# Kernel optimization log

Hardware: AMD Instinct MI355X
Metric: run time of the kernel (lower is better)

## Reference

```python
import jax, jax.numpy as jnp
import numpy as np

HIDDEN = 1024
HEADS = 16
HEAD_DIM = HIDDEN // HEADS


def setup_inputs() -> dict:
    key = jax.random.key(0)
    ks = jax.random.split(key, 7)
    B, S, H = 8, 1024, HIDDEN
    hidden_states = jax.random.normal(ks[0], (B, S, H), dtype=jnp.float32)
    attention_mask = jnp.zeros((B, 1, 1, S), dtype=jnp.float32)
    # Xavier-uniform weights [out, in], zero biases (matches module init)
    limit = float(np.sqrt(6.0 / (H + H)))
    Wq = jax.random.uniform(ks[1], (H, H), minval=-limit, maxval=limit, dtype=jnp.float32)
    Wk = jax.random.uniform(ks[2], (H, H), minval=-limit, maxval=limit, dtype=jnp.float32)
    Wv = jax.random.uniform(ks[3], (H, H), minval=-limit, maxval=limit, dtype=jnp.float32)
    bq = jnp.zeros((H,), dtype=jnp.float32)
    bk = jnp.zeros((H,), dtype=jnp.float32)
    bv = jnp.zeros((H,), dtype=jnp.float32)
    return {"hidden_states": hidden_states, "attention_mask": attention_mask,
            "Wq": Wq, "bq": bq, "Wk": Wk, "bk": bk, "Wv": Wv, "bv": bv}


def _split_heads(x):
    # [B, S, H] -> [B, heads, S, head_dim]
    B, S, _ = x.shape
    return x.reshape(B, S, HEADS, HEAD_DIM).transpose(0, 2, 1, 3)


def reference(hidden_states, attention_mask, Wq, bq, Wk, bk, Wv, bv):
    # Linear projections: y = x @ W^T + b  (weights stored [out, in] as in torch)
    q = _split_heads(hidden_states @ Wq.T + bq)
    k = _split_heads(hidden_states @ Wk.T + bk)
    v = _split_heads(hidden_states @ Wv.T + bv)
    scale = 1.0 / (HEAD_DIM ** 0.5)
    scores = jnp.einsum('bhqd,bhkd->bhqk', q, k) * scale  # [B,heads,S,S]
    scores = scores + attention_mask
    probs = jax.nn.softmax(scores, axis=-1)
    # dropout is identity at inference
    ctx = jnp.einsum('bhqk,bhkd->bhqd', probs, v)
    B, _, S, _ = ctx.shape
    return ctx.transpose(0, 2, 1, 3).reshape(B, S, HIDDEN)
```

## Files before the change

kernel.cpp:

```cpp
#include <hip/hip_runtime.h>
#include <hip/hip_bf16.h>
#include <stdint.h>

#define B_ 8
#define S_ 1024
#define NH_ 16
#define D_ 64
#define H_ 1024
#define M_TOT (B_*S_)
#define LOG2E 1.44269504088896f

typedef __attribute__((ext_vector_type(8))) short short8;
typedef __attribute__((ext_vector_type(4))) float f32x4;
typedef __attribute__((ext_vector_type(16))) float f32x16;

#if __has_builtin(__builtin_amdgcn_exp2f)
#define EXP2(x) __builtin_amdgcn_exp2f(x)
#else
#define EXP2(x) __expf((x) * 0.69314718056f)
#endif

static __device__ __forceinline__ unsigned short f2bf(float f) {
  union { float f; unsigned u; } c; c.f = f;
  unsigned u = c.u;
  return (unsigned short)((u + 0x7fffu + ((u >> 16) & 1u)) >> 16);
}

static __device__ __forceinline__ void gld_lds16(void* lds, const void* g) {
  __builtin_amdgcn_global_load_lds((const __attribute__((address_space(1))) unsigned*)g,
                                   (__attribute__((address_space(3))) unsigned*)lds, 16, 0, 0);
}

#define WAIT_LGKM0() asm volatile("s_waitcnt lgkmcnt(0)" ::: "memory")
#define WAIT_VM(n)   asm volatile("s_waitcnt vmcnt(" #n ")" ::: "memory")
#define SBAR()       __builtin_amdgcn_s_barrier()
#define SCHED0()     __builtin_amdgcn_sched_barrier(0)

__global__ void cvt_f32_bf16(const float* __restrict__ X,
                             const float* __restrict__ Wq,
                             const float* __restrict__ Wk,
                             const float* __restrict__ Wv,
                             unsigned short* __restrict__ Xbf,
                             unsigned short* __restrict__ Wbf) {
  const long long NX = (long long)M_TOT * H_;
  const long long NW = (long long)H_ * H_;
  long long t = (long long)blockIdx.x * blockDim.x + threadIdx.x;
  const long long stride = (long long)gridDim.x * blockDim.x;
  const long long total4 = (NX + 3 * NW) >> 2;
  for (; t < total4; t += stride) {
    long long e = t << 2;
    const float* src; unsigned short* dst;
    if (e < NX) { src = X + e; dst = Xbf + e; }
    else {
      long long r = e - NX;
      int w = (int)(r / NW);
      long long o = r - (long long)w * NW;
      src = (w == 0 ? Wq : (w == 1 ? Wk : Wv)) + o;
      dst = Wbf + (long long)w * NW + o;
    }
    float4 v = *(const float4*)src;
    ushort4 u;
    u.x = f2bf(v.x); u.y = f2bf(v.y); u.z = f2bf(v.z); u.w = f2bf(v.w);
    *(ushort4*)dst = u;
  }
}

#define QBM 128
#define QBN 256
#define QBK 64
#define BUFSZ 49152

__global__ __launch_bounds__(512, 2) void qkv_gemm(
    const unsigned short* __restrict__ Xbf,
    const unsigned short* __restrict__ Wbf,
    const float* __restrict__ bq, const float* __restrict__ bk,
    const float* __restrict__ bv,
    unsigned short* __restrict__ Qo, unsigned short* __restrict__ Ko,
    unsigned short* __restrict__ Vt) {
  __shared__ char lds[3 * BUFSZ];

  const int tid = threadIdx.x;
  const int w = tid >> 6;
  const int l = tid & 63;
  const int lrow = l & 15, lgrp = l >> 4;
  const int wm = w >> 2, wn = w & 3;

  const int orig = blockIdx.x;
  const int xcd = orig & 7;
  const int slot = orig >> 3;
  const int z = slot >> 5;
  const int i = slot & 31;
  const int mtile = (xcd * 8 + (i >> 2)) * QBM;
  const int ntile = (i & 3) * QBN;

  const unsigned short* Wz = Wbf + (long long)z * H_ * H_;

  const int srow = l >> 3;
  const int sslot = l & 7;
  auto stageA = [&](char* buf, int j, int k0) {
    int row = j * 8 + srow;
    int so = (sslot ^ (row & 7)) * 8;
    gld_lds16(buf + j * 1024, Xbf + (long long)(mtile + row) * H_ + k0 + so);
  };
  auto stageB = [&](char* buf, int j, int k0) {
    int row = j * 8 + srow;
    int so = (sslot ^ (row & 7)) * 8;
    gld_lds16(buf + 16384 + j * 1024, Wz + (long long)(ntile + row) * H_ + k0 + so);
  };

  const int strA = (z == 2 ? wn : wm) * 64;
  const int strB = (z == 2 ? wm : wn) * 64;
  const int offA = (z == 2) ? 16384 : 0;
  const int offB = (z == 2) ? 0 : 16384;
  auto rdA = [&](char* buf, int fi, int ks) -> short8 {
    int r = strA + fi * 16 + lrow;
    return *(const short8*)(buf + offA + r * 128 + (((ks * 4 + lgrp) ^ (r & 7)) * 16));
  };
  auto rdB = [&](char* buf, int fi, int ks) -> short8 {
    int r = strB + fi * 16 + lrow;
    return *(const short8*)(buf + offB + r * 128 + (((ks * 4 + lgrp) ^ (r & 7)) * 16));
  };

  f32x4 acc[4][4];
  f32x4 zero = {0.f, 0.f, 0.f, 0.f};
  #pragma unroll
  for (int a = 0; a < 4; ++a)
    #pragma unroll
    for (int c = 0; c < 4; ++c) acc[a][c] = zero;

  {
    char* b0p = lds;
    char* b1p = lds + BUFSZ;
    stageA(b0p, 2 * w + 0, 0); stageA(b0p, 2 * w + 1, 0);
    #pragma unroll
    for (int c = 0; c < 4; ++c) stageB(b0p, 4 * w + c, 0);
    stageA(b1p, 2 * w + 0, QBK); stageA(b1p, 2 * w + 1, QBK);
    #pragma unroll
    for (int c = 0; c < 4; ++c) stageB(b1p, 4 * w + c, QBK);
  }
  WAIT_VM(6);
  SBAR();

  #pragma unroll 1
  for (int t = 0; t < 16; ++t) {
    char* buf  = lds + (t % 3) * BUFSZ;
    char* nbuf = lds + ((t + 2) % 3) * BUFSZ;
    const int k0n = (t + 2) * QBK;
    const bool st = (t + 2 < 16);

    short8 af[4][2], bf[2][2];

    #pragma unroll
    for (int fi = 0; fi < 4; ++fi)
      #pragma unroll
      for (int ks = 0; ks < 2; ++ks) af[fi][ks] = rdA(buf, fi, ks);
    #pragma unroll
    for (int fi = 0; fi < 2; ++fi)
      #pragma unroll
      for (int ks = 0; ks < 2; ++ks) bf[fi][ks] = rdB(buf, fi, ks);
    if (st) { stageA(nbuf, 2 * w + 0, k0n); stageA(nbuf, 2 * w + 1, k0n);
              stageB(nbuf, 4 * w + 0, k0n); }
    SBAR();
    WAIT_LGKM0(); SCHED0();
    __builtin_amdgcn_s_setprio(1);
    #pragma unroll
    for (int im = 0; im < 4; ++im)
      #pragma unroll
      for (int in = 0; in < 2; ++in)
        #pragma unroll
        for (int ks = 0; ks < 2; ++ks)
          acc[im][in] = __builtin_amdgcn_mfma_f32_16x16x32_bf16(
              af[im][ks], bf[in][ks], acc[im][in], 0, 0, 0);
    __builtin_amdgcn_s_setprio(0);
    SBAR();

    #pragma unroll
    for (int fi = 0; fi < 2; ++fi)
      #pragma unroll
      for (int ks = 0; ks < 2; ++ks) bf[fi][ks] = rdB(buf, 2 + fi, ks);
    if (st) { stageB(nbuf, 4 * w + 1, k0n); stageB(nbuf, 4 * w + 2, k0n);
              stageB(nbuf, 4 * w + 3, k0n); }
    SBAR();
    WAIT_LGKM0(); SCHED0();
    __builtin_amdgcn_s_setprio(1);
    #pragma unroll
    for (int im = 0; im < 4; ++im)
      #pragma unroll
      for (int in = 0; in < 2; ++in)
        #pragma unroll
        for (int ks = 0; ks < 2; ++ks)
          acc[im][2 + in] = __builtin_amdgcn_mfma_f32_16x16x32_bf16(
              af[im][ks], bf[in][ks], acc[im][2 + in], 0, 0, 0);
    __builtin_amdgcn_s_setprio(0);
    if (t < 14) { WAIT_VM(6); } else { WAIT_VM(0); }
    SBAR();
  }

  const float* bias = (z == 0) ? bq : (z == 1) ? bk : bv;
  if (z != 2) {
    unsigned short* O = (z == 0) ? Qo : Ko;
    #pragma unroll
    for (int in = 0; in < 4; ++in) {
      int n = ntile + wn * 64 + in * 16 + lrow;
      float bv_ = bias[n];
      int h = n >> 6, d = n & 63;
      #pragma unroll
      for (int im = 0; im < 4; ++im)
        #pragma unroll
        for (int r = 0; r < 4; ++r) {
          int m = mtile + wm * 64 + im * 16 + lgrp * 4 + r;
          float val = acc[im][in][r] + bv_;
          if (z == 0) val *= 0.125f * LOG2E;
          int b = m >> 10, s = m & 1023;
          O[(((long long)(b * NH_ + h)) * S_ + s) * D_ + d] = f2bf(val);
        }
    }
  } else {
    #pragma unroll
    for (int im = 0; im < 4; ++im)
      #pragma unroll
      for (int r = 0; r < 4; ++r) {
        int nfull = ntile + wn * 64 + im * 16 + lgrp * 4 + r;
        float bv_ = bias[nfull];
        int h = nfull >> 6, d = nfull & 63;
        #pragma unroll
        for (int in = 0; in < 4; ++in) {
          int mfull = mtile + wm * 64 + in * 16 + lrow;
          float val = acc[im][in][r] + bv_;
          int b = mfull >> 10, s = mfull & 1023;
          Vt[(((long long)(b * NH_ + h)) * D_ + d) * S_ + s] = f2bf(val);
        }
      }
  }
}

__global__ __launch_bounds__(256, 2) void attn_fused(
    const unsigned short* __restrict__ Qbf,
    const unsigned short* __restrict__ Kbf,
    const unsigned short* __restrict__ Vtb,
    const float* __restrict__ mask,
    float* __restrict__ out) {
  __shared__ char lds[32768];
  const int tid = threadIdx.x, w = tid >> 6, l = tid & 63;
  const int l31 = l & 31, h = l >> 5;

  const int lid = blockIdx.x;
  const int xcd = lid & 7, k8 = lid >> 3;
  const int bh = xcd * 16 + (k8 >> 2);
  const int qt = k8 & 3;
  const int b = bh >> 4, hd = bh & 15;
  const int q0 = qt * 256 + w * 64;

  const unsigned short* Kg = Kbf + (long long)bh * S_ * D_;
  const unsigned short* Vg = Vtb + (long long)bh * D_ * S_;
  const float* mrow = mask + b * S_;

  {
    const int row = (w * 2) * 8 + (l >> 3);
    const int row1 = (w * 2 + 1) * 8 + (l >> 3);
    const int so = ((l & 7) ^ (row & 7)) * 8;
    const int so1 = ((l & 7) ^ (row1 & 7)) * 8;
    gld_lds16(lds + (w * 2) * 1024,        Kg + (long long)row * D_ + so);
    gld_lds16(lds + (w * 2 + 1) * 1024,    Kg + (long long)row1 * D_ + so1);
    gld_lds16(lds + 8192 + (w * 2) * 1024, Vg + (long long)row * S_ + so);
    gld_lds16(lds + 8192 + (w * 2 + 1) * 1024, Vg + (long long)row1 * S_ + so1);
  }

  short8 qf[2][4];
  #pragma unroll
  for (int qb = 0; qb < 2; ++qb)
    #pragma unroll
    for (int ks = 0; ks < 4; ++ks)
      qf[qb][ks] = *(const short8*)(Qbf + ((long long)bh * S_ + q0 + qb * 32 + l31) * D_ + ks * 16 + 8 * h);

  f32x16 acc[2][2];
  #pragma unroll
  for (int db = 0; db < 2; ++db)
    #pragma unroll
    for (int qb = 0; qb < 2; ++qb)
      #pragma unroll
      for (int r = 0; r < 16; ++r) acc[db][qb][r] = 0.f;
  float m_run[2] = {-1e30f, -1e30f};
  float l_run[2] = {0.f, 0.f};

  __syncthreads();

  for (int kt = 0; kt < S_ / 64; ++kt) {
    const int p = kt & 1;
    char* ldsK = lds + p * 16384;
    char* ldsV = ldsK + 8192;
    const int key0 = kt * 64;

    if (kt < S_ / 64 - 1) {
      char* nb = lds + (p ^ 1) * 16384;
      const int nk0 = key0 + 64;
      #pragma unroll
      for (int t = 0; t < 2; ++t) {
        int j = w * 2 + t;
        int row = j * 8 + (l >> 3);
        int so = ((l & 7) ^ (row & 7)) * 8;
        gld_lds16(nb + j * 1024,        Kg + (long long)(nk0 + row) * D_ + so);
        gld_lds16(nb + 8192 + j * 1024, Vg + (long long)row * S_ + nk0 + so);
      }
    }

    f32x16 sc[2][2];
    #pragma unroll
    for (int kb = 0; kb < 2; ++kb)
      #pragma unroll
      for (int qb = 0; qb < 2; ++qb)
        #pragma unroll
        for (int r = 0; r < 16; ++r) sc[kb][qb][r] = 0.f;

    #pragma unroll
    for (int kb = 0; kb < 2; ++kb) {
      short8 kf[4];
      #pragma unroll
      for (int ks = 0; ks < 4; ++ks) {
        int row = kb * 32 + l31;
        int g = (2 * ks + h) ^ (row & 7);
        kf[ks] = *(const short8*)(ldsK + row * 128 + g * 16);
      }
      __builtin_amdgcn_s_setprio(1);
      #pragma unroll
      for (int qb = 0; qb < 2; ++qb)
        #pragma unroll
        for (int ks = 0; ks < 4; ++ks)
          sc[kb][qb] = __builtin_amdgcn_mfma_f32_32x32x16_bf16(
              kf[ks], qf[qb][ks], sc[kb][qb], 0, 0, 0);
      __builtin_amdgcn_s_setprio(0);
    }

    short8 pfrag[2][4];
    #pragma unroll
    for (int qb = 0; qb < 2; ++qb) {
      float sv[32];
      #pragma unroll
      for (int kb = 0; kb < 2; ++kb)
        #pragma unroll
        for (int rg = 0; rg < 4; ++rg) {
          f32x4 m4 = *(const f32x4*)(mrow + key0 + kb * 32 + rg * 8 + 4 * h);
          #pragma unroll
          for (int c = 0; c < 4; ++c)
            sv[kb * 16 + rg * 4 + c] = fmaf(m4[c], LOG2E, sc[kb][qb][rg * 4 + c]);
        }
      float r16[16];
      #pragma unroll
      for (int i = 0; i < 16; ++i) r16[i] = fmaxf(sv[i], sv[i + 16]);
      #pragma unroll
      for (int i = 0; i < 8; ++i) r16[i] = fmaxf(r16[i], r16[i + 8]);
      #pragma unroll
      for (int i = 0; i < 4; ++i) r16[i] = fmaxf(r16[i], r16[i + 4]);
      float pm = fmaxf(fmaxf(r16[0], r16[1]), fmaxf(r16[2], r16[3]));
      pm = fmaxf(pm, __shfl_xor(pm, 32));
      if (!__all(pm - m_run[qb] <= 11.5f)) {
        float mn = fmaxf(m_run[qb], pm);
        float rs = EXP2(m_run[qb] - mn);
        m_run[qb] = mn;
        l_run[qb] *= rs;
        #pragma unroll
        for (int db = 0; db < 2; ++db)
          #pragma unroll
          for (int r = 0; r < 16; ++r) acc[db][qb][r] *= rs;
      }
      const float mcur = m_run[qb];
      #pragma unroll
      for (int i = 0; i < 32; ++i) sv[i] = EXP2(sv[i] - mcur);
      #pragma unroll
      for (int i = 0; i < 16; ++i) r16[i] = sv[i] + sv[i + 16];
      #pragma unroll
      for (int i = 0; i < 8; ++i) r16[i] = r16[i] + r16[i + 8];
      #pragma unroll
      for (int i = 0; i < 4; ++i) r16[i] = r16[i] + r16[i + 4];
      float ps = (r16[0] + r16[1]) + (r16[2] + r16[3]);
      ps += __shfl_xor(ps, 32);
      l_run[qb] += ps;

      unsigned Wd[8][2];
      #pragma unroll
      for (int j = 0; j < 8; ++j) {
        int base = (j >> 2) * 16 + (j & 3) * 4;
        asm("v_cvt_pk_bf16_f32 %0, %1, %2" : "=v"(Wd[j][0]) : "v"(sv[base + 0]), "v"(sv[base + 1]));
        asm("v_cvt_pk_bf16_f32 %0, %1, %2" : "=v"(Wd[j][1]) : "v"(sv[base + 2]), "v"(sv[base + 3]));
      }
      #pragma unroll
      for (int ks = 0; ks < 4; ++ks) {
        unsigned s0 = h ? Wd[2 * ks][0] : Wd[2 * ks + 1][0];
        unsigned s1 = h ? Wd[2 * ks][1] : Wd[2 * ks + 1][1];
        unsigned r0 = __shfl_xor(s0, 32);
        unsigned r1 = __shfl_xor(s1, 32);
        unsigned o0 = h ? Wd[2 * ks + 1][0] : Wd[2 * ks][0];
        unsigned o1 = h ? Wd[2 * ks + 1][1] : Wd[2 * ks][1];
        union { unsigned u[4]; short8 s; } fu;
        fu.u[0] = h ? r0 : o0;
        fu.u[1] = h ? r1 : o1;
        fu.u[2] = h ? o0 : r0;
        fu.u[3] = h ? o1 : r1;
        pfrag[qb][ks] = fu.s;
      }
    }

    #pragma unroll
    for (int db = 0; db < 2; ++db) {
      short8 vf[4];
      #pragma unroll
      for (int ks = 0; ks < 4; ++ks) {
        int row = db * 32 + l31;
        int g = (2 * ks + h) ^ (row & 7);
        vf[ks] = *(const short8*)(ldsV + row * 128 + g * 16);
      }
      __builtin_amdgcn_s_setprio(1);
      #pragma unroll
      for (int qb = 0; qb < 2; ++qb)
        #pragma unroll
        for (int ks = 0; ks < 4; ++ks)
          acc[db][qb] = __builtin_amdgcn_mfma_f32_32x32x16_bf16(
              vf[ks], pfrag[qb][ks], acc[db][qb], 0, 0, 0);
      __builtin_amdgcn_s_setprio(0);
    }

    __syncthreads();
  }

  #pragma unroll
  for (int qb = 0; qb < 2; ++qb) {
    float inv = 1.0f / l_run[qb];
    int q = q0 + qb * 32 + l31;
    float* orow = out + ((long long)b * S_ + q) * H_ + hd * D_;
    #pragma unroll
    for (int db = 0; db < 2; ++db)
      #pragma unroll
      for (int rg = 0; rg < 4; ++rg) {
        f32x4 v4;
        #pragma unroll
        for (int c = 0; c < 4; ++c) v4[c] = acc[db][qb][rg * 4 + c] * inv;
        *(f32x4*)(orow + db * 32 + rg * 8 + 4 * h) = v4;
      }
  }
}

extern "C" void kernel_launch(void* const* d_in, const int* in_sizes, int n_in,
                              void* d_out, int out_size, void* d_ws, size_t ws_size,
                              hipStream_t stream) {
  const float* X    = (const float*)d_in[0];
  const float* mask = (const float*)d_in[1];
  const float* Wq   = (const float*)d_in[2];
  const float* bq   = (const float*)d_in[3];
  const float* Wk   = (const float*)d_in[4];
  const float* bk   = (const float*)d_in[5];
  const float* Wv   = (const float*)d_in[6];
  const float* bv   = (const float*)d_in[7];
  float* out = (float*)d_out;

  char* ws = (char*)d_ws;
  unsigned short* Xbf = (unsigned short*)ws;
  unsigned short* Wbf = (unsigned short*)(ws + 16777216);
  unsigned short* Qb  = (unsigned short*)(ws + 23068672);
  unsigned short* Kb  = (unsigned short*)(ws + 39845888);
  unsigned short* Vt  = (unsigned short*)(ws + 56623104);

  hipLaunchKernelGGL(cvt_f32_bf16, dim3(2048), dim3(256), 0, stream,
                     X, Wq, Wk, Wv, Xbf, Wbf);
  hipLaunchKernelGGL(qkv_gemm, dim3(768), dim3(512), 0, stream,
                     Xbf, Wbf, bq, bk, bv, Qb, Kb, Vt);
  hipLaunchKernelGGL(attn_fused, dim3(512), dim3(256), 0, stream,
                     Qb, Kb, Vt, mask, out);
}
```

Measured before the change: 132.6 us.

## Enlarge QKV GEMM tile to 256x256 with double-buffered register-prefetch pipeline

The QKV projection GEMM tile grows from 128x256 to 256x256, so each wave owns 128x64 outputs and the grid halves to 384 blocks. The LDS pipeline goes from triple to double buffering, and the next tile's A and B fragments are prefetched into registers while MFMAs run, using partial lgkmcnt waits. The aim is more reuse per LDS byte and less barrier stall per MFMA. In exchange it doubles the accumulator registers, which can hurt occupancy under launch_bounds(512,2), and leaves fewer blocks to balance across the CUs.

```diff
diff --git a/kernel.cpp b/kernel.cpp
--- a/kernel.cpp
+++ b/kernel.cpp
@@ -31,10 +31,13 @@
                                    (__attribute__((address_space(3))) unsigned*)lds, 16, 0, 0);
 }
 
-#define WAIT_LGKM0() asm volatile("s_waitcnt lgkmcnt(0)" ::: "memory")
-#define WAIT_VM(n)   asm volatile("s_waitcnt vmcnt(" #n ")" ::: "memory")
-#define SBAR()       __builtin_amdgcn_s_barrier()
-#define SCHED0()     __builtin_amdgcn_sched_barrier(0)
+#define WAIT_LGKM(n)  asm volatile("s_waitcnt lgkmcnt(" #n ")" ::: "memory")
+#define WAIT_LGKM0()  asm volatile("s_waitcnt lgkmcnt(0)" ::: "memory")
+#define WAIT_VM(n)    asm volatile("s_waitcnt vmcnt(" #n ")" ::: "memory")
+#define SBAR()        __builtin_amdgcn_s_barrier()
+#define SCHED0()      __builtin_amdgcn_sched_barrier(0)
+#define PRIO1()       __builtin_amdgcn_s_setprio(1)
+#define PRIO0()       __builtin_amdgcn_s_setprio(0)
 
 __global__ void cvt_f32_bf16(const float* __restrict__ X,
                              const float* __restrict__ Wq,
@@ -65,10 +68,11 @@
   }
 }
 
-#define QBM 128
+#define QBM 256
 #define QBN 256
 #define QBK 64
-#define BUFSZ 49152
+#define ABYTES 32768
+#define BUFSZ  65536
 
 __global__ __launch_bounds__(512, 2) void qkv_gemm(
     const unsigned short* __restrict__ Xbf,
@@ -77,7 +81,7 @@
     const float* __restrict__ bv,
     unsigned short* __restrict__ Qo, unsigned short* __restrict__ Ko,
     unsigned short* __restrict__ Vt) {
-  __shared__ char lds[3 * BUFSZ];
+  __shared__ char lds[2 * BUFSZ];
 
   const int tid = threadIdx.x;
   const int w = tid >> 6;
@@ -88,10 +92,10 @@
   const int orig = blockIdx.x;
   const int xcd = orig & 7;
   const int slot = orig >> 3;
-  const int z = slot >> 5;
-  const int i = slot & 31;
-  const int mtile = (xcd * 8 + (i >> 2)) * QBM;
-  const int ntile = (i & 3) * QBN;
+  const int nz = slot >> 2;
+  const int mtile = (xcd * 4 + (slot & 3)) * QBM;
+  const int ntile = (nz & 3) * QBN;
+  const int z = nz >> 2;
 
   const unsigned short* Wz = Wbf + (long long)z * H_ * H_;
 
@@ -105,13 +109,13 @@
   auto stageB = [&](char* buf, int j, int k0) {
     int row = j * 8 + srow;
     int so = (sslot ^ (row & 7)) * 8;
-    gld_lds16(buf + 16384 + j * 1024, Wz + (long long)(ntile + row) * H_ + k0 + so);
-  };
-
-  const int strA = (z == 2 ? wn : wm) * 64;
-  const int strB = (z == 2 ? wm : wn) * 64;
-  const int offA = (z == 2) ? 16384 : 0;
-  const int offB = (z == 2) ? 0 : 16384;
+    gld_lds16(buf + ABYTES + j * 1024, Wz + (long long)(ntile + row) * H_ + k0 + so);
+  };
+
+  const int strA = wm * 128;
+  const int strB = wn * 64;
+  const int offA = (z == 2) ? ABYTES : 0;
+  const int offB = (z == 2) ? 0 : ABYTES;
   auto rdA = [&](char* buf, int fi, int ks) -> short8 {
     int r = strA + fi * 16 + lrow;
     return *(const short8*)(buf + offA + r * 128 + (((ks * 4 + lgrp) ^ (r & 7)) * 16));
@@ -121,79 +125,89 @@
     return *(const short8*)(buf + offB + r * 128 + (((ks * 4 + lgrp) ^ (r & 7)) * 16));
   };
 
-  f32x4 acc[4][4];
+  f32x4 acc[8][4];
   f32x4 zero = {0.f, 0.f, 0.f, 0.f};
   #pragma unroll
-  for (int a = 0; a < 4; ++a)
+  for (int a = 0; a < 8; ++a)
     #pragma unroll
     for (int c = 0; c < 4; ++c) acc[a][c] = zero;
 
-  {
-    char* b0p = lds;
-    char* b1p = lds + BUFSZ;
-    stageA(b0p, 2 * w + 0, 0); stageA(b0p, 2 * w + 1, 0);
-    #pragma unroll
-    for (int c = 0; c < 4; ++c) stageB(b0p, 4 * w + c, 0);
-    stageA(b1p, 2 * w + 0, QBK); stageA(b1p, 2 * w + 1, QBK);
-    #pragma unroll
-    for (int c = 0; c < 4; ++c) stageB(b1p, 4 * w + c, QBK);
-  }
-  WAIT_VM(6);
+  short8 afA[4][2], afB[4][2], bfC[2][2], bfN[2][2];
+
+  auto mmq = [&](int i0, int j0, short8 (&AF)[4][2], short8 (&BF)[2][2]) {
+    #pragma unroll
+    for (int a = 0; a < 4; ++a)
+      #pragma unroll
+      for (int b = 0; b < 2; ++b)
+        #pragma unroll
+        for (int ks = 0; ks < 2; ++ks)
+          acc[i0 + a][j0 + b] = __builtin_amdgcn_mfma_f32_16x16x32_bf16(
+              AF[a][ks], BF[b][ks], acc[i0 + a][j0 + b], 0, 0, 0);
+  };
+
+  auto tile_body = [&](char* buf, char* nbuf, int k0n, bool st,
+                       short8 (&af0)[4][2], short8 (&af1)[4][2]) {
+    #pragma unroll
+    for (int fi = 0; fi < 4; ++fi)
+      #pragma unroll
+      for (int ks = 0; ks < 2; ++ks) af1[fi][ks] = rdA(buf, 4 + fi, ks);
+    if (st) {
+      stageA(nbuf, w * 4 + 0, k0n); stageA(nbuf, w * 4 + 1, k0n);
+      stageA(nbuf, w * 4 + 2, k0n); stageA(nbuf, w * 4 + 3, k0n);
+    }
+    SBAR();
+    WAIT_LGKM(8); SCHED0();
+    PRIO1(); mmq(0, 0, af0, bfC); PRIO0();
+
+    #pragma unroll
+    for (int fi = 0; fi < 2; ++fi)
+      #pragma unroll
+      for (int ks = 0; ks < 2; ++ks) bfN[fi][ks] = rdB(buf, 2 + fi, ks);
+    if (st) {
+      stageB(nbuf, w * 4 + 0, k0n); stageB(nbuf, w * 4 + 1, k0n);
+      stageB(nbuf, w * 4 + 2, k0n); stageB(nbuf, w * 4 + 3, k0n);
+    }
+    SBAR();
+    WAIT_LGKM(4); SCHED0();
+    PRIO1(); mmq(4, 0, af1, bfC); PRIO0();
+
+    WAIT_LGKM0(); SCHED0();
+    PRIO1(); mmq(4, 2, af1, bfN); PRIO0();
+    WAIT_VM(0);
+    SBAR();
+
+    if (st) {
+      #pragma unroll
+      for (int fi = 0; fi < 4; ++fi)
+        #pragma unroll
+        for (int ks = 0; ks < 2; ++ks) af1[fi][ks] = rdA(nbuf, fi, ks);
+      #pragma unroll
+      for (int fi = 0; fi < 2; ++fi)
+        #pragma unroll
+        for (int ks = 0; ks < 2; ++ks) bfC[fi][ks] = rdB(nbuf, fi, ks);
+    }
+    PRIO1(); mmq(0, 2, af0, bfN); PRIO0();
+  };
+
+  #pragma unroll
+  for (int c = 0; c < 4; ++c) stageA(lds, w * 4 + c, 0);
+  #pragma unroll
+  for (int c = 0; c < 4; ++c) stageB(lds, w * 4 + c, 0);
+  WAIT_VM(0);
   SBAR();
+  #pragma unroll
+  for (int fi = 0; fi < 4; ++fi)
+    #pragma unroll
+    for (int ks = 0; ks < 2; ++ks) afA[fi][ks] = rdA(lds, fi, ks);
+  #pragma unroll
+  for (int fi = 0; fi < 2; ++fi)
+    #pragma unroll
+    for (int ks = 0; ks < 2; ++ks) bfC[fi][ks] = rdB(lds, fi, ks);
 
   #pragma unroll 1
-  for (int t = 0; t < 16; ++t) {
-    char* buf  = lds + (t % 3) * BUFSZ;
-    char* nbuf = lds + ((t + 2) % 3) * BUFSZ;
-    const int k0n = (t + 2) * QBK;
-    const bool st = (t + 2 < 16);
-
-    short8 af[4][2], bf[2][2];
-
-    #pragma unroll
-    for (int fi = 0; fi < 4; ++fi)
-      #pragma unroll
-      for (int ks = 0; ks < 2; ++ks) af[fi][ks] = rdA(buf, fi, ks);
-    #pragma unroll
-    for (int fi = 0; fi < 2; ++fi)
-      #pragma unroll
-      for (int ks = 0; ks < 2; ++ks) bf[fi][ks] = rdB(buf, fi, ks);
-    if (st) { stageA(nbuf, 2 * w + 0, k0n); stageA(nbuf, 2 * w + 1, k0n);
-              stageB(nbuf, 4 * w + 0, k0n); }
-    SBAR();
-    WAIT_LGKM0(); SCHED0();
-    __builtin_amdgcn_s_setprio(1);
-    #pragma unroll
-    for (int im = 0; im < 4; ++im)
-      #pragma unroll
-      for (int in = 0; in < 2; ++in)
-        #pragma unroll
-        for (int ks = 0; ks < 2; ++ks)
-          acc[im][in] = __builtin_amdgcn_mfma_f32_16x16x32_bf16(
-              af[im][ks], bf[in][ks], acc[im][in], 0, 0, 0);
-    __builtin_amdgcn_s_setprio(0);
-    SBAR();
-
-    #pragma unroll
-    for (int fi = 0; fi < 2; ++fi)
-      #pragma unroll
-      for (int ks = 0; ks < 2; ++ks) bf[fi][ks] = rdB(buf, 2 + fi, ks);
-    if (st) { stageB(nbuf, 4 * w + 1, k0n); stageB(nbuf, 4 * w + 2, k0n);
-              stageB(nbuf, 4 * w + 3, k0n); }
-    SBAR();
-    WAIT_LGKM0(); SCHED0();
-    __builtin_amdgcn_s_setprio(1);
-    #pragma unroll
-    for (int im = 0; im < 4; ++im)
-      #pragma unroll
-      for (int in = 0; in < 2; ++in)
-        #pragma unroll
-        for (int ks = 0; ks < 2; ++ks)
-          acc[im][2 + in] = __builtin_amdgcn_mfma_f32_16x16x32_bf16(
-              af[im][ks], bf[in][ks], acc[im][2 + in], 0, 0, 0);
-    __builtin_amdgcn_s_setprio(0);
-    if (t < 14) { WAIT_VM(6); } else { WAIT_VM(0); }
-    SBAR();
+  for (int t = 0; t < 16; t += 2) {
+    tile_body(lds,          lds + BUFSZ, (t + 1) * QBK, true,        afA, afB);
+    tile_body(lds + BUFSZ,  lds,         (t + 2) * QBK, (t + 2) < 16, afB, afA);
   }
 
   const float* bias = (z == 0) ? bq : (z == 1) ? bk : bv;
@@ -205,10 +219,10 @@
       float bv_ = bias[n];
       int h = n >> 6, d = n & 63;
       #pragma unroll
-      for (int im = 0; im < 4; ++im)
+      for (int im = 0; im < 8; ++im)
         #pragma unroll
         for (int r = 0; r < 4; ++r) {
-          int m = mtile + wm * 64 + im * 16 + lgrp * 4 + r;
+          int m = mtile + wm * 128 + im * 16 + lgrp * 4 + r;
           float val = acc[im][in][r] + bv_;
           if (z == 0) val *= 0.125f * LOG2E;
           int b = m >> 10, s = m & 1023;
@@ -217,15 +231,15 @@
     }
   } else {
     #pragma unroll
-    for (int im = 0; im < 4; ++im)
+    for (int im = 0; im < 8; ++im)
       #pragma unroll
       for (int r = 0; r < 4; ++r) {
-        int nfull = ntile + wn * 64 + im * 16 + lgrp * 4 + r;
+        int nfull = ntile + wm * 128 + im * 16 + lgrp * 4 + r;
         float bv_ = bias[nfull];
         int h = nfull >> 6, d = nfull & 63;
         #pragma unroll
         for (int in = 0; in < 4; ++in) {
-          int mfull = mtile + wm * 64 + in * 16 + lrow;
+          int mfull = mtile + wn * 64 + in * 16 + lrow;
           float val = acc[im][in][r] + bv_;
           int b = mfull >> 10, s = mfull & 1023;
           Vt[(((long long)(b * NH_ + h)) * D_ + d) * S_ + s] = f2bf(val);
@@ -461,7 +475,7 @@
 
   hipLaunchKernelGGL(cvt_f32_bf16, dim3(2048), dim3(256), 0, stream,
                      X, Wq, Wk, Wv, Xbf, Wbf);
-  hipLaunchKernelGGL(qkv_gemm, dim3(768), dim3(512), 0, stream,
+  hipLaunchKernelGGL(qkv_gemm, dim3(384), dim3(512), 0, stream,
                      Xbf, Wbf, bq, bk, bv, Qb, Kb, Vt);
   hipLaunchKernelGGL(attn_fused, dim3(512), dim3(256), 0, stream,
                      Qb, Kb, Vt, mask, out);
```

Measured after the change: 192.5 us. +45.1%, slower.

## Triple-buffer K/V staging and cache attention mask row in LDS

Applied to the files above, without the earlier changes.

Switches the attention kernel's K/V LDS staging from a double buffer to a triple buffer with a prefetch distance of two tiles. Explicit vmcnt waits let one tile's loads stay in flight across the barrier. It also loads the batch's mask row into LDS once, so the inner loop reads the mask from LDS instead of global memory. LDS use grows from 32 KB to 52 KB per block, which may limit how many blocks fit on a CU under the launch bound of 2.

```diff
diff --git a/kernel.cpp b/kernel.cpp
--- a/kernel.cpp
+++ b/kernel.cpp
@@ -240,7 +240,8 @@
     const unsigned short* __restrict__ Vtb,
     const float* __restrict__ mask,
     float* __restrict__ out) {
-  __shared__ char lds[32768];
+  __shared__ char lds[3 * 16384 + 4096];
+  char* ldsM = lds + 49152;
   const int tid = threadIdx.x, w = tid >> 6, l = tid & 63;
   const int l31 = l & 31, h = l >> 5;
 
@@ -255,16 +256,17 @@
   const unsigned short* Vg = Vtb + (long long)bh * D_ * S_;
   const float* mrow = mask + b * S_;
 
-  {
-    const int row = (w * 2) * 8 + (l >> 3);
-    const int row1 = (w * 2 + 1) * 8 + (l >> 3);
-    const int so = ((l & 7) ^ (row & 7)) * 8;
-    const int so1 = ((l & 7) ^ (row1 & 7)) * 8;
-    gld_lds16(lds + (w * 2) * 1024,        Kg + (long long)row * D_ + so);
-    gld_lds16(lds + (w * 2 + 1) * 1024,    Kg + (long long)row1 * D_ + so1);
-    gld_lds16(lds + 8192 + (w * 2) * 1024, Vg + (long long)row * S_ + so);
-    gld_lds16(lds + 8192 + (w * 2 + 1) * 1024, Vg + (long long)row1 * S_ + so1);
-  }
+  auto stageKV = [&](int kt, char* buf) {
+    const int key0 = kt * 64;
+    #pragma unroll
+    for (int t = 0; t < 2; ++t) {
+      int j = w * 2 + t;
+      int row = j * 8 + (l >> 3);
+      int so = ((l & 7) ^ (row & 7)) * 8;
+      gld_lds16(buf + j * 1024,        Kg + (long long)(key0 + row) * D_ + so);
+      gld_lds16(buf + 8192 + j * 1024, Vg + (long long)row * S_ + key0 + so);
+    }
+  };
 
   short8 qf[2][4];
   #pragma unroll
@@ -272,6 +274,13 @@
     #pragma unroll
     for (int ks = 0; ks < 4; ++ks)
       qf[qb][ks] = *(const short8*)(Qbf + ((long long)bh * S_ + q0 + qb * 32 + l31) * D_ + ks * 16 + 8 * h);
+  gld_lds16(ldsM + w * 1024, mrow + w * 256 + l * 4);
+  SCHED0(); WAIT_VM(0); SCHED0();
+
+  stageKV(0, lds);
+  stageKV(1, lds + 16384);
+  SCHED0(); WAIT_VM(4); SCHED0();
+  SBAR();
 
   f32x16 acc[2][2];
   #pragma unroll
@@ -283,26 +292,14 @@
   float m_run[2] = {-1e30f, -1e30f};
   float l_run[2] = {0.f, 0.f};
 
-  __syncthreads();
-
+  #pragma unroll 1
   for (int kt = 0; kt < S_ / 64; ++kt) {
-    const int p = kt & 1;
-    char* ldsK = lds + p * 16384;
+    char* ldsK = lds + (kt % 3) * 16384;
     char* ldsV = ldsK + 8192;
     const int key0 = kt * 64;
-
-    if (kt < S_ / 64 - 1) {
-      char* nb = lds + (p ^ 1) * 16384;
-      const int nk0 = key0 + 64;
-      #pragma unroll
-      for (int t = 0; t < 2; ++t) {
-        int j = w * 2 + t;
-        int row = j * 8 + (l >> 3);
-        int so = ((l & 7) ^ (row & 7)) * 8;
-        gld_lds16(nb + j * 1024,        Kg + (long long)(nk0 + row) * D_ + so);
-        gld_lds16(nb + 8192 + j * 1024, Vg + (long long)row * S_ + nk0 + so);
-      }
-    }
+    const bool st = (kt + 2 < S_ / 64);
+
+    if (st) stageKV(kt + 2, lds + ((kt + 2) % 3) * 16384);
 
     f32x16 sc[2][2];
     #pragma unroll
@@ -339,7 +336,7 @@
       for (int kb = 0; kb < 2; ++kb)
         #pragma unroll
         for (int rg = 0; rg < 4; ++rg) {
-          f32x4 m4 = *(const f32x4*)(mrow + key0 + kb * 32 + rg * 8 + 4 * h);
+          f32x4 m4 = *(const f32x4*)(ldsM + (key0 + kb * 32 + rg * 8 + 4 * h) * 4);
           #pragma unroll
           for (int c = 0; c < 4; ++c)
             sv[kb * 16 + rg * 4 + c] = fmaf(m4[c], LOG2E, sc[kb][qb][rg * 4 + c]);
@@ -419,7 +416,9 @@
       __builtin_amdgcn_s_setprio(0);
     }
 
-    __syncthreads();
+    if (st) { SCHED0(); WAIT_VM(4); SCHED0(); }
+    else if (kt + 1 < S_ / 64) { SCHED0(); WAIT_VM(0); SCHED0(); }
+    SBAR();
   }
 
   #pragma unroll
```

New measurement: 133.0 us. Within noise of the previous version (+0.3%).
